# Kernel tuning notes

Hardware: AMD Instinct MI355X
Metric: run time of the kernel (lower is better)

Reference implementation:

```python
import jax, jax.numpy as jnp
import numpy as np
from jax import lax


def _leaky(x):
    # LeakyReLU, negative_slope=0.1
    return jnp.where(x > 0, x, 0.1 * x)


def _conv(x, w, pad, groups=1):
    # NCHW / OIHW 2D conv, stride 1
    return lax.conv_general_dilated(
        x, w, (1, 1), [(pad, pad), (pad, pad)],
        dimension_numbers=("NCHW", "OIHW", "NCHW"),
        feature_group_count=groups)


def setup_inputs() -> dict:
    key = jax.random.key(0)
    ks = jax.random.split(key, 12)
    B, C, H, W = 16, 64, 256, 256
    KS = 3

    def nrm(k, shape, fan_in):
        return jax.random.normal(k, shape, jnp.float32) / np.float32(np.sqrt(fan_in))

    return {
        "x": jax.random.normal(ks[0], (B, C, H, W), jnp.float32),
        "t": jax.random.normal(ks[1], (B, 1, 1, 1), jnp.float32),
        # t_process: 1x1 convs (1->64, 64->64), no bias -> stored as matrices
        "tW1": nrm(ks[2], (C, 1), 1),
        "tW2": nrm(ks[3], (C, C), C),
        # f_process: two 3x3 convs 64->64 with bias
        "fW1": nrm(ks[4], (C, C, KS, KS), C * KS * KS),
        "fb1": jnp.zeros((C,), jnp.float32),
        "fW2": nrm(ks[5], (C, C, KS, KS), C * KS * KS),
        "fb2": jnp.zeros((C,), jnp.float32),
        # kernel branch: 1x1 convs (1->64, 64->64*9), no bias
        "kW1": nrm(ks[6], (C, 1), 1),
        "kW2": nrm(ks[7], (C * KS * KS, C), C),
        # conv33: 3x3 conv 64->64 with bias
        "cW": nrm(ks[8], (C, C, KS, KS), C * KS * KS),
        "cb": jnp.zeros((C,), jnp.float32),
    }


def reference(x, t, tW1, tW2, fW1, fb1, fW2, fb2, kW1, kW2, cW, cb):
    b, c, h, w = x.shape
    KS = 3

    # f_process: Conv3x3 -> LeakyReLU -> Conv3x3 -> LeakyReLU
    f = _leaky(_conv(x, fW1, 1) + fb1[None, :, None, None])
    f = _leaky(_conv(f, fW2, 1) + fb2[None, :, None, None])

    # t is (b,1,1,1); 1x1 convs on it are per-sample matmuls
    ts = t.reshape(b, 1)
    # t_process: Conv1x1 -> LeakyReLU -> Conv1x1 -> Sigmoid -> (b,c,1,1)
    mv = jax.nn.sigmoid(_leaky(ts @ tW1.T) @ tW2.T).reshape(b, c, 1, 1)

    # kernel branch: Conv1x1 -> LeakyReLU -> Conv1x1 -> LeakyReLU -> (b*c,1,3,3)
    kern = _leaky(_leaky(ts @ kW1.T) @ kW2.T).reshape(b * c, 1, KS, KS)

    # per-sample-channel dynamic depthwise conv: groups = b*c
    out = _conv(f.reshape(1, b * c, h, w), kern, (KS - 1) // 2,
                groups=b * c).reshape(b, c, h, w)

    # modulation gating + residual 3x3 conv
    return out * mv + _conv(x, cW, 1) + cb[None, :, None, None]
```

## Files before the change

kernel.cpp:

```cpp
#include <hip/hip_runtime.h>
#include <cstdint>

using short8  = __attribute__((ext_vector_type(8))) short;
using short4v = __attribute__((ext_vector_type(4))) short;
using f32x16  = __attribute__((ext_vector_type(16))) float;
using float4v = __attribute__((ext_vector_type(4))) float;
typedef unsigned short ushort_t;

__device__ __forceinline__ float lrelu(float x) { return x > 0.f ? x : 0.1f * x; }

__device__ __forceinline__ ushort_t f2bf(float f) {
    union { float f; unsigned u; } v; v.f = f;
    unsigned r = (v.u + 0x7FFFu + ((v.u >> 16) & 1u)) >> 16;
    return (ushort_t)r;
}
__device__ __forceinline__ float bf2f(ushort_t b) {
    union { unsigned u; float f; } v; v.u = ((unsigned)b) << 16; return v.f;
}

__device__ __forceinline__ void gload_lds16(const ushort_t* g, ushort_t* l) {
    __builtin_amdgcn_global_load_lds(
        (const __attribute__((address_space(1))) void*)g,
        (__attribute__((address_space(3))) void*)l, 16, 0, 0);
}

__global__ void k_tiny(const float* __restrict__ t, const float* __restrict__ tW1,
                       const float* __restrict__ tW2, const float* __restrict__ kW1,
                       const float* __restrict__ kW2, float* __restrict__ ktr) {
    int b = blockIdx.x;
    int c = threadIdx.x;
    __shared__ float h1[64], g1[64];
    float ts = t[b];
    h1[c] = lrelu(ts * tW1[c]);
    g1[c] = lrelu(ts * kW1[c]);
    __syncthreads();
    float s = 0.f;
    for (int j = 0; j < 64; ++j) s = fmaf(tW2[c * 64 + j], h1[j], s);
    float mvv = 1.f / (1.f + expf(-s));
    for (int q = 0; q < 9; ++q) {
        float s2 = 0.f;
        for (int j = 0; j < 64; ++j) s2 = fmaf(kW2[(c * 9 + q) * 64 + j], g1[j], s2);
        ktr[b * 576 + q * 64 + c] = lrelu(s2) * mvv;
    }
}

__global__ void k_zrow(ushort_t* __restrict__ z) {
    int i = blockIdx.x * 256 + threadIdx.x;
    *(short8*)(z + (size_t)i * 8) = (short8)0;
}

__global__ void k_pack(const float* __restrict__ w1, const float* __restrict__ w2,
                       const float* __restrict__ w3, ushort_t* __restrict__ wp) {
    int idx = blockIdx.x * 256 + threadIdx.x;
    if (idx >= 3 * 36864) return;
    int conv = idx / 36864, r = idx % 36864;
    const float* W = conv == 0 ? w1 : (conv == 1 ? w2 : w3);
    int j = r & 7, lane = (r >> 3) & 63, ct = (r >> 9) & 1, kc = (r >> 10) & 1,
        ch = (r >> 11) & 1, t = r >> 12;
    int co = ct * 32 + (lane & 31);
    int ci = ch * 32 + kc * 16 + (lane >> 5) * 8 + j;
    wp[idx] = f2bf(W[(co * 64 + ci) * 9 + t]);
}

__global__ __launch_bounds__(256) void k_tr(const float* __restrict__ x,
                                            ushort_t* __restrict__ xbf) {
    int bid = blockIdx.x;
    int h = bid & 255, b = bid >> 8;
    int t = threadIdx.x;
    for (int it = 0; it < 8; ++it) {
        int idx = t + it * 256;
        int g = idx & 7, w = idx >> 3;
        const float* src = x + (((size_t)(b * 64 + g * 8) * 256 + h) * 256 + w);
        short8 v;
#pragma unroll
        for (int j = 0; j < 8; ++j) v[j] = (short)f2bf(src[(size_t)j * 65536]);
        *(short8*)(xbf + (((size_t)(b * 256 + h) * 256 + w) * 64 + g * 8)) = v;
    }
}

template <bool LEAKY, int OMODE>
__global__ __launch_bounds__(256, 3) void k_conv(const ushort_t* __restrict__ in,
                                                 const ushort_t* __restrict__ zv,
                                                 const ushort_t* __restrict__ wp,
                                                 const float* __restrict__ bias,
                                                 void* __restrict__ outp) {
    __shared__ __align__(16) ushort_t xs[3136 * 8];
    const int tid = threadIdx.x;
    const int lane = tid & 63;
    const int wv = tid >> 6;
    const unsigned bid = blockIdx.x;
    const unsigned L = (bid & 7u) * 512u + (bid >> 3);
    const int h = L & 255, b = L >> 8;
    const int l31 = lane & 31, lhi = lane >> 5;
    const int pw0 = wv * 64;

    const ushort_t* rb0 = (h > 0)   ? in + ((size_t)(b * 256 + h - 1)) * 16384 : zv;
    const ushort_t* rb1 =             in + ((size_t)(b * 256 + h)) * 16384;
    const ushort_t* rb2 = (h < 255) ? in + ((size_t)(b * 256 + h + 1)) * 16384 : zv;

    f32x16 acc[2][2];
#pragma unroll
    for (int a = 0; a < 2; ++a)
#pragma unroll
        for (int c = 0; c < 2; ++c) acc[a][c] = (f32x16)0.0f;

    for (int ch = 0; ch < 2; ++ch) {
        __syncthreads();
#pragma unroll
        for (int it = 0; it < 13; ++it) {
            int base = it * 256 + wv * 64;
            if (base < 3120) {
                int S = base + lane;
                S = S < 3120 ? S : 3119;
                int r = (S >= 2080) ? 2 : (S >= 1040 ? 1 : 0);
                int rem = S - r * 1040;
                int m = rem >> 3, sl = rem & 7;
                int sp = sl ^ (m & 7);
                int p = 2 * m + (sp >> 2), g = sp & 3;
                int ws = p - 1;
                bool edge = (unsigned)ws >= 256u;
                const ushort_t* rp = (r == 0) ? rb0 : (r == 1 ? rb1 : rb2);
                const ushort_t* src =
                    edge ? zv : (rp + ws * 64 + ch * 32 + g * 8);
                gload_lds16(src, xs + (size_t)base * 8);
            }
        }
        asm volatile("s_waitcnt vmcnt(0)" ::: "memory");
        __syncthreads();

#pragma unroll
        for (int t = 0; t < 9; ++t) {
            const int dw = t % 3;
#pragma unroll
            for (int kc = 0; kc < 2; ++kc) {
                const ushort_t* wpf = wp + (((((t * 2 + ch) * 2 + kc) * 2) * 64 + lane) * 8);
                short8 a0 = *(const short8*)(wpf);
                short8 a1 = *(const short8*)(wpf + 512);
                const int g = kc * 2 + lhi;
                const int rr = t / 3;
#pragma unroll
                for (int pt = 0; pt < 2; ++pt) {
                    int p = pw0 + pt * 32 + l31 + dw;
                    int slot = ((p & 1) * 4 + g) ^ ((p >> 1) & 7);
                    short8 bf = *(const short8*)(xs + (((size_t)rr * 130 + (p >> 1)) * 8 + slot) * 8);
                    acc[0][pt] = __builtin_amdgcn_mfma_f32_32x32x16_bf16(a0, bf, acc[0][pt], 0, 0, 0);
                    acc[1][pt] = __builtin_amdgcn_mfma_f32_32x32x16_bf16(a1, bf, acc[1][pt], 0, 0, 0);
                }
            }
        }
    }

    const int co_b = 4 * lhi;
    if (OMODE == 0) {
        ushort_t* outb = (ushort_t*)outp + ((size_t)(b * 256 + h)) * 16384;
#pragma unroll
        for (int ct = 0; ct < 2; ++ct)
#pragma unroll
            for (int pt = 0; pt < 2; ++pt) {
                int pix = pw0 + pt * 32 + l31;
                ushort_t* po = outb + (size_t)pix * 64 + ct * 32 + co_b;
#pragma unroll
                for (int q = 0; q < 4; ++q) {
                    float4v bv = *(const float4v*)(bias + ct * 32 + co_b + 8 * q);
                    short4v sv;
#pragma unroll
                    for (int m = 0; m < 4; ++m) {
                        float v = acc[ct][pt][q * 4 + m] + bv[m];
                        if (LEAKY) v = lrelu(v);
                        sv[m] = (short)f2bf(v);
                    }
                    *(short4v*)(po + 8 * q) = sv;
                }
            }
    } else if (OMODE == 1) {
        ushort_t* pb = (ushort_t*)outp + (((size_t)b * 64) << 16) + h * 256;
#pragma unroll
        for (int ct = 0; ct < 2; ++ct)
#pragma unroll
            for (int pt = 0; pt < 2; ++pt) {
                int pix = pw0 + pt * 32 + l31;
#pragma unroll
                for (int q = 0; q < 4; ++q) {
                    float4v bv = *(const float4v*)(bias + ct * 32 + co_b + 8 * q);
#pragma unroll
                    for (int m = 0; m < 4; ++m) {
                        int c = ct * 32 + co_b + 8 * q + m;
                        float v = acc[ct][pt][q * 4 + m] + bv[m];
                        if (LEAKY) v = lrelu(v);
                        pb[((size_t)c << 16) + pix] = f2bf(v);
                    }
                }
            }
    } else {
        float* pb = (float*)outp + (((size_t)b * 64) << 16) + h * 256;
#pragma unroll
        for (int ct = 0; ct < 2; ++ct)
#pragma unroll
            for (int pt = 0; pt < 2; ++pt) {
                int pix = pw0 + pt * 32 + l31;
#pragma unroll
                for (int q = 0; q < 4; ++q) {
                    float4v bv = *(const float4v*)(bias + ct * 32 + co_b + 8 * q);
#pragma unroll
                    for (int m = 0; m < 4; ++m) {
                        int c = ct * 32 + co_b + 8 * q + m;
                        float v = acc[ct][pt][q * 4 + m] + bv[m];
                        if (LEAKY) v = lrelu(v);
                        pb[((size_t)c << 16) + pix] = v;
                    }
                }
            }
    }
}

__global__ __launch_bounds__(256) void k_fin(const ushort_t* __restrict__ f2,
                                             const float* __restrict__ ktr,
                                             float* __restrict__ out) {
    __shared__ __align__(16) ushort_t s[10 * 272];
    const unsigned bid = blockIdx.x;
    const unsigned L = (bid & 7u) * 4096u + (bid >> 3);
    const int hb = L & 31, c = (L >> 5) & 63, b = L >> 11;
    const int h0 = hb * 8;
    const int w = threadIdx.x;

    const ushort_t* f2c = f2 + (((size_t)(b * 64 + c)) << 16);
    for (int i = w; i < 320; i += 256) {
        int r = i >> 5, seg = i & 31;
        int hs = h0 - 1 + r;
        short8 v = (short8)0;
        if ((unsigned)hs < 256u) v = *(const short8*)(f2c + hs * 256 + seg * 8);
        *(short8*)(&s[r * 272 + 8 + seg * 8]) = v;
        if (seg == 0) s[r * 272 + 7] = 0;
        if (seg == 31) s[r * 272 + 264] = 0;
    }
    __syncthreads();

    float kv[9];
#pragma unroll
    for (int t9 = 0; t9 < 9; ++t9) kv[t9] = ktr[b * 576 + t9 * 64 + c];

    float lv[10], cv[10], rv[10];
#pragma unroll
    for (int r = 0; r < 10; ++r) {
        lv[r] = bf2f(s[r * 272 + 7 + w]);
        cv[r] = bf2f(s[r * 272 + 8 + w]);
        rv[r] = bf2f(s[r * 272 + 9 + w]);
    }

    float* ob = out + (((size_t)(b * 64 + c)) << 16) + h0 * 256 + w;
#pragma unroll
    for (int rr = 0; rr < 8; ++rr) {
        float dwv = 0.f;
#pragma unroll
        for (int r3 = 0; r3 < 3; ++r3) {
            dwv = fmaf(kv[r3 * 3 + 0], lv[rr + r3], dwv);
            dwv = fmaf(kv[r3 * 3 + 1], cv[rr + r3], dwv);
            dwv = fmaf(kv[r3 * 3 + 2], rv[rr + r3], dwv);
        }
        float* po = ob + rr * 256;
        *po = *po + dwv;
    }
}

extern "C" void kernel_launch(void* const* d_in, const int* in_sizes, int n_in,
                              void* d_out, int out_size, void* d_ws, size_t ws_size,
                              hipStream_t stream) {
    const float* x   = (const float*)d_in[0];
    const float* t   = (const float*)d_in[1];
    const float* tW1 = (const float*)d_in[2];
    const float* tW2 = (const float*)d_in[3];
    const float* fW1 = (const float*)d_in[4];
    const float* fb1 = (const float*)d_in[5];
    const float* fW2 = (const float*)d_in[6];
    const float* fb2 = (const float*)d_in[7];
    const float* kW1 = (const float*)d_in[8];
    const float* kW2 = (const float*)d_in[9];
    const float* cW  = (const float*)d_in[10];
    const float* cb  = (const float*)d_in[11];

    char* ws = (char*)d_ws;
    float*    ktr  = (float*)ws;
    ushort_t* wp   = (ushort_t*)(ws + 65536);
    ushort_t* zv   = (ushort_t*)(ws + 294912);
    ushort_t* xbf  = (ushort_t*)(ws + (512u << 10));
    ushort_t* f2n  = (ushort_t*)(ws + (512u << 10) + ((size_t)128 << 20));
    ushort_t* f1bf = (ushort_t*)d_out;
    float*    out  = (float*)d_out;

    k_tiny<<<dim3(16), dim3(64), 0, stream>>>(t, tW1, tW2, kW1, kW2, ktr);
    k_zrow<<<dim3(8), dim3(256), 0, stream>>>(zv);
    k_pack<<<dim3((3 * 36864 + 255) / 256), dim3(256), 0, stream>>>(fW1, fW2, cW, wp);
    k_tr<<<dim3(4096), dim3(256), 0, stream>>>(x, xbf);

    k_conv<true, 0><<<dim3(4096), dim3(256), 0, stream>>>(xbf, zv, wp, fb1, (void*)f1bf);
    k_conv<true, 1><<<dim3(4096), dim3(256), 0, stream>>>(f1bf, zv, wp + 36864, fb2, (void*)f2n);
    k_conv<false, 2><<<dim3(4096), dim3(256), 0, stream>>>(xbf, zv, wp + 2 * 36864, cb, (void*)out);
    k_fin<<<dim3(32768), dim3(256), 0, stream>>>(f2n, ktr, out);
}
```

Measured before the change: 673.9 us.

## Fuse first f-conv and residual conv into one kernel sharing input tile

The first f_process conv and the residual conv33 both read the same bf16 input x, so they are merged into one kernel that stages the input tile in LDS once and runs both weight sets' MFMAs against it. This removes one full kernel launch and one full pass of input loads. The price is doubled accumulator registers (32 more f32x16 worth), which may lower occupancy under the launch bound of 3 blocks per SM or cause spills. Buffers are reassigned so f1 goes to workspace and f2 reuses the xbf buffer, since out now receives the residual early.

```diff
diff --git a/kernel.cpp b/kernel.cpp
--- a/kernel.cpp
+++ b/kernel.cpp
@@ -78,12 +78,11 @@
     }
 }
 
-template <bool LEAKY, int OMODE>
-__global__ __launch_bounds__(256, 3) void k_conv(const ushort_t* __restrict__ in,
-                                                 const ushort_t* __restrict__ zv,
-                                                 const ushort_t* __restrict__ wp,
-                                                 const float* __restrict__ bias,
-                                                 void* __restrict__ outp) {
+__global__ __launch_bounds__(256, 3) void k_conv13(
+    const ushort_t* __restrict__ in, const ushort_t* __restrict__ zv,
+    const ushort_t* __restrict__ wpa, const ushort_t* __restrict__ wpc,
+    const float* __restrict__ ba, const float* __restrict__ bc,
+    ushort_t* __restrict__ f1out, float* __restrict__ cres) {
     __shared__ __align__(16) ushort_t xs[3136 * 8];
     const int tid = threadIdx.x;
     const int lane = tid & 63;
@@ -98,11 +97,11 @@
     const ushort_t* rb1 =             in + ((size_t)(b * 256 + h)) * 16384;
     const ushort_t* rb2 = (h < 255) ? in + ((size_t)(b * 256 + h + 1)) * 16384 : zv;
 
-    f32x16 acc[2][2];
+    f32x16 accA[2][2], accC[2][2];
 #pragma unroll
     for (int a = 0; a < 2; ++a)
 #pragma unroll
-        for (int c = 0; c < 2; ++c) acc[a][c] = (f32x16)0.0f;
+        for (int c = 0; c < 2; ++c) { accA[a][c] = (f32x16)0.0f; accC[a][c] = (f32x16)0.0f; }
 
     for (int ch = 0; ch < 2; ++ch) {
         __syncthreads();
@@ -120,8 +119,7 @@
                 int ws = p - 1;
                 bool edge = (unsigned)ws >= 256u;
                 const ushort_t* rp = (r == 0) ? rb0 : (r == 1 ? rb1 : rb2);
-                const ushort_t* src =
-                    edge ? zv : (rp + ws * 64 + ch * 32 + g * 8);
+                const ushort_t* src = edge ? zv : (rp + ws * 64 + ch * 32 + g * 8);
                 gload_lds16(src, xs + (size_t)base * 8);
             }
         }
@@ -131,13 +129,129 @@
 #pragma unroll
         for (int t = 0; t < 9; ++t) {
             const int dw = t % 3;
+            const int rr = t / 3;
+#pragma unroll
+            for (int kc = 0; kc < 2; ++kc) {
+                const int off = ((((t * 2 + ch) * 2 + kc) * 2) * 64 + lane) * 8;
+                short8 a0 = *(const short8*)(wpa + off);
+                short8 a1 = *(const short8*)(wpa + off + 512);
+                short8 c0 = *(const short8*)(wpc + off);
+                short8 c1 = *(const short8*)(wpc + off + 512);
+                const int g = kc * 2 + lhi;
+#pragma unroll
+                for (int pt = 0; pt < 2; ++pt) {
+                    int p = pw0 + pt * 32 + l31 + dw;
+                    int slot = ((p & 1) * 4 + g) ^ ((p >> 1) & 7);
+                    short8 bf = *(const short8*)(xs + (((size_t)rr * 130 + (p >> 1)) * 8 + slot) * 8);
+                    accA[0][pt] = __builtin_amdgcn_mfma_f32_32x32x16_bf16(a0, bf, accA[0][pt], 0, 0, 0);
+                    accA[1][pt] = __builtin_amdgcn_mfma_f32_32x32x16_bf16(a1, bf, accA[1][pt], 0, 0, 0);
+                    accC[0][pt] = __builtin_amdgcn_mfma_f32_32x32x16_bf16(c0, bf, accC[0][pt], 0, 0, 0);
+                    accC[1][pt] = __builtin_amdgcn_mfma_f32_32x32x16_bf16(c1, bf, accC[1][pt], 0, 0, 0);
+                }
+            }
+        }
+    }
+
+    const int co_b = 4 * lhi;
+    {
+        ushort_t* outb = f1out + ((size_t)(b * 256 + h)) * 16384;
+#pragma unroll
+        for (int ct = 0; ct < 2; ++ct)
+#pragma unroll
+            for (int pt = 0; pt < 2; ++pt) {
+                int pix = pw0 + pt * 32 + l31;
+                ushort_t* po = outb + (size_t)pix * 64 + ct * 32 + co_b;
+#pragma unroll
+                for (int q = 0; q < 4; ++q) {
+                    float4v bv = *(const float4v*)(ba + ct * 32 + co_b + 8 * q);
+                    short4v sv;
+#pragma unroll
+                    for (int m = 0; m < 4; ++m) {
+                        float v = lrelu(accA[ct][pt][q * 4 + m] + bv[m]);
+                        sv[m] = (short)f2bf(v);
+                    }
+                    *(short4v*)(po + 8 * q) = sv;
+                }
+            }
+    }
+    {
+        float* pb = cres + (((size_t)b * 64) << 16) + h * 256;
+#pragma unroll
+        for (int ct = 0; ct < 2; ++ct)
+#pragma unroll
+            for (int pt = 0; pt < 2; ++pt) {
+                int pix = pw0 + pt * 32 + l31;
+#pragma unroll
+                for (int q = 0; q < 4; ++q) {
+                    float4v bv = *(const float4v*)(bc + ct * 32 + co_b + 8 * q);
+#pragma unroll
+                    for (int m = 0; m < 4; ++m) {
+                        int c = ct * 32 + co_b + 8 * q + m;
+                        pb[((size_t)c << 16) + pix] = accC[ct][pt][q * 4 + m] + bv[m];
+                    }
+                }
+            }
+    }
+}
+
+__global__ __launch_bounds__(256, 3) void k_conv2(const ushort_t* __restrict__ in,
+                                                  const ushort_t* __restrict__ zv,
+                                                  const ushort_t* __restrict__ wp,
+                                                  const float* __restrict__ bias,
+                                                  ushort_t* __restrict__ outp) {
+    __shared__ __align__(16) ushort_t xs[3136 * 8];
+    const int tid = threadIdx.x;
+    const int lane = tid & 63;
+    const int wv = tid >> 6;
+    const unsigned bid = blockIdx.x;
+    const unsigned L = (bid & 7u) * 512u + (bid >> 3);
+    const int h = L & 255, b = L >> 8;
+    const int l31 = lane & 31, lhi = lane >> 5;
+    const int pw0 = wv * 64;
+
+    const ushort_t* rb0 = (h > 0)   ? in + ((size_t)(b * 256 + h - 1)) * 16384 : zv;
+    const ushort_t* rb1 =             in + ((size_t)(b * 256 + h)) * 16384;
+    const ushort_t* rb2 = (h < 255) ? in + ((size_t)(b * 256 + h + 1)) * 16384 : zv;
+
+    f32x16 acc[2][2];
+#pragma unroll
+    for (int a = 0; a < 2; ++a)
+#pragma unroll
+        for (int c = 0; c < 2; ++c) acc[a][c] = (f32x16)0.0f;
+
+    for (int ch = 0; ch < 2; ++ch) {
+        __syncthreads();
+#pragma unroll
+        for (int it = 0; it < 13; ++it) {
+            int base = it * 256 + wv * 64;
+            if (base < 3120) {
+                int S = base + lane;
+                S = S < 3120 ? S : 3119;
+                int r = (S >= 2080) ? 2 : (S >= 1040 ? 1 : 0);
+                int rem = S - r * 1040;
+                int m = rem >> 3, sl = rem & 7;
+                int sp = sl ^ (m & 7);
+                int p = 2 * m + (sp >> 2), g = sp & 3;
+                int ws = p - 1;
+                bool edge = (unsigned)ws >= 256u;
+                const ushort_t* rp = (r == 0) ? rb0 : (r == 1 ? rb1 : rb2);
+                const ushort_t* src = edge ? zv : (rp + ws * 64 + ch * 32 + g * 8);
+                gload_lds16(src, xs + (size_t)base * 8);
+            }
+        }
+        asm volatile("s_waitcnt vmcnt(0)" ::: "memory");
+        __syncthreads();
+
+#pragma unroll
+        for (int t = 0; t < 9; ++t) {
+            const int dw = t % 3;
+            const int rr = t / 3;
 #pragma unroll
             for (int kc = 0; kc < 2; ++kc) {
                 const ushort_t* wpf = wp + (((((t * 2 + ch) * 2 + kc) * 2) * 64 + lane) * 8);
                 short8 a0 = *(const short8*)(wpf);
                 short8 a1 = *(const short8*)(wpf + 512);
                 const int g = kc * 2 + lhi;
-                const int rr = t / 3;
 #pragma unroll
                 for (int pt = 0; pt < 2; ++pt) {
                     int p = pw0 + pt * 32 + l31 + dw;
@@ -151,66 +265,23 @@
     }
 
     const int co_b = 4 * lhi;
-    if (OMODE == 0) {
-        ushort_t* outb = (ushort_t*)outp + ((size_t)(b * 256 + h)) * 16384;
-#pragma unroll
-        for (int ct = 0; ct < 2; ++ct)
-#pragma unroll
-            for (int pt = 0; pt < 2; ++pt) {
-                int pix = pw0 + pt * 32 + l31;
-                ushort_t* po = outb + (size_t)pix * 64 + ct * 32 + co_b;
-#pragma unroll
-                for (int q = 0; q < 4; ++q) {
-                    float4v bv = *(const float4v*)(bias + ct * 32 + co_b + 8 * q);
-                    short4v sv;
-#pragma unroll
-                    for (int m = 0; m < 4; ++m) {
-                        float v = acc[ct][pt][q * 4 + m] + bv[m];
-                        if (LEAKY) v = lrelu(v);
-                        sv[m] = (short)f2bf(v);
-                    }
-                    *(short4v*)(po + 8 * q) = sv;
-                }
-            }
-    } else if (OMODE == 1) {
-        ushort_t* pb = (ushort_t*)outp + (((size_t)b * 64) << 16) + h * 256;
-#pragma unroll
-        for (int ct = 0; ct < 2; ++ct)
-#pragma unroll
-            for (int pt = 0; pt < 2; ++pt) {
-                int pix = pw0 + pt * 32 + l31;
-#pragma unroll
-                for (int q = 0; q < 4; ++q) {
-                    float4v bv = *(const float4v*)(bias + ct * 32 + co_b + 8 * q);
-#pragma unroll
-                    for (int m = 0; m < 4; ++m) {
-                        int c = ct * 32 + co_b + 8 * q + m;
-                        float v = acc[ct][pt][q * 4 + m] + bv[m];
-                        if (LEAKY) v = lrelu(v);
-                        pb[((size_t)c << 16) + pix] = f2bf(v);
-                    }
-                }
-            }
-    } else {
-        float* pb = (float*)outp + (((size_t)b * 64) << 16) + h * 256;
-#pragma unroll
-        for (int ct = 0; ct < 2; ++ct)
-#pragma unroll
-            for (int pt = 0; pt < 2; ++pt) {
-                int pix = pw0 + pt * 32 + l31;
-#pragma unroll
-                for (int q = 0; q < 4; ++q) {
-                    float4v bv = *(const float4v*)(bias + ct * 32 + co_b + 8 * q);
-#pragma unroll
-                    for (int m = 0; m < 4; ++m) {
-                        int c = ct * 32 + co_b + 8 * q + m;
-                        float v = acc[ct][pt][q * 4 + m] + bv[m];
-                        if (LEAKY) v = lrelu(v);
-                        pb[((size_t)c << 16) + pix] = v;
-                    }
-                }
-            }
-    }
+    ushort_t* pb = outp + (((size_t)b * 64) << 16) + h * 256;
+#pragma unroll
+    for (int ct = 0; ct < 2; ++ct)
+#pragma unroll
+        for (int pt = 0; pt < 2; ++pt) {
+            int pix = pw0 + pt * 32 + l31;
+#pragma unroll
+            for (int q = 0; q < 4; ++q) {
+                float4v bv = *(const float4v*)(bias + ct * 32 + co_b + 8 * q);
+#pragma unroll
+                for (int m = 0; m < 4; ++m) {
+                    int c = ct * 32 + co_b + 8 * q + m;
+                    float v = lrelu(acc[ct][pt][q * 4 + m] + bv[m]);
+                    pb[((size_t)c << 16) + pix] = f2bf(v);
+                }
+            }
+        }
 }
 
 __global__ __launch_bounds__(256) void k_fin(const ushort_t* __restrict__ f2,
@@ -283,8 +354,8 @@
     ushort_t* wp   = (ushort_t*)(ws + 65536);
     ushort_t* zv   = (ushort_t*)(ws + 294912);
     ushort_t* xbf  = (ushort_t*)(ws + (512u << 10));
-    ushort_t* f2n  = (ushort_t*)(ws + (512u << 10) + ((size_t)128 << 20));
-    ushort_t* f1bf = (ushort_t*)d_out;
+    ushort_t* f1bf = (ushort_t*)(ws + (512u << 10) + ((size_t)128 << 20));
+    ushort_t* f2n  = xbf;
     float*    out  = (float*)d_out;
 
     k_tiny<<<dim3(16), dim3(64), 0, stream>>>(t, tW1, tW2, kW1, kW2, ktr);
@@ -292,8 +363,8 @@
     k_pack<<<dim3((3 * 36864 + 255) / 256), dim3(256), 0, stream>>>(fW1, fW2, cW, wp);
     k_tr<<<dim3(4096), dim3(256), 0, stream>>>(x, xbf);
 
-    k_conv<true, 0><<<dim3(4096), dim3(256), 0, stream>>>(xbf, zv, wp, fb1, (void*)f1bf);
-    k_conv<true, 1><<<dim3(4096), dim3(256), 0, stream>>>(f1bf, zv, wp + 36864, fb2, (void*)f2n);
-    k_conv<false, 2><<<dim3(4096), dim3(256), 0, stream>>>(xbf, zv, wp + 2 * 36864, cb, (void*)out);
+    k_conv13<<<dim3(4096), dim3(256), 0, stream>>>(
+        xbf, zv, wp, wp + 2 * 36864, fb1, cb, f1bf, out);
+    k_conv2<<<dim3(4096), dim3(256), 0, stream>>>(f1bf, zv, wp + 36864, fb2, f2n);
     k_fin<<<dim3(32768), dim3(256), 0, stream>>>(f2n, ktr, out);
 }
```

Result: slower. 716.1 us (+6.3%).

## Restructure conv into 2-row blocks with LDS weights, double-buffered staging, fused depthwise

Applied to the files above, without the earlier changes.

The conv kernel now uses 512-thread blocks that each compute two output rows. All weights are staged into LDS once per block, and the input channels are split into four 16-channel chunks loaded into a double-buffered LDS ring, so global loads overlap the MFMA work. The separate depthwise/final kernel is removed and its dynamic 3x3 depthwise conv is fused into the residual conv epilogue, which reads f2 directly from global memory. The cost is roughly 140KB of dynamic LDS per block, which limits occupancy, plus uncoalesced scattered f2 reads in the epilogue.

```diff
diff --git a/kernel.cpp b/kernel.cpp
--- a/kernel.cpp
+++ b/kernel.cpp
@@ -7,6 +7,13 @@
 using float4v = __attribute__((ext_vector_type(4))) float;
 typedef unsigned short ushort_t;
 
+#define CROW 520
+#define CSLOTS 2080
+#define BSLOTS 2144
+#define BSH (BSLOTS * 8)
+#define WSH 36864
+#define DYN_LDS ((WSH + 2 * BSH) * 2)
+
 __device__ __forceinline__ float lrelu(float x) { return x > 0.f ? x : 0.1f * x; }
 
 __device__ __forceinline__ ushort_t f2bf(float f) {
@@ -23,6 +30,10 @@
         (const __attribute__((address_space(1))) void*)g,
         (__attribute__((address_space(3))) void*)l, 16, 0, 0);
 }
+
+#define VMCNT(n) asm volatile("s_waitcnt vmcnt(" #n ")" ::: "memory")
+#define RBAR() __builtin_amdgcn_s_barrier()
+#define SCHED0() __builtin_amdgcn_sched_barrier(0)
 
 __global__ void k_tiny(const float* __restrict__ t, const float* __restrict__ tW1,
                        const float* __restrict__ tW2, const float* __restrict__ kW1,
@@ -55,10 +66,10 @@
     if (idx >= 3 * 36864) return;
     int conv = idx / 36864, r = idx % 36864;
     const float* W = conv == 0 ? w1 : (conv == 1 ? w2 : w3);
-    int j = r & 7, lane = (r >> 3) & 63, ct = (r >> 9) & 1, kc = (r >> 10) & 1,
-        ch = (r >> 11) & 1, t = r >> 12;
+    int j = r & 7, lane = (r >> 3) & 63, ct = (r >> 9) & 1, chunk = (r >> 10) & 3,
+        t = r >> 12;
     int co = ct * 32 + (lane & 31);
-    int ci = ch * 32 + kc * 16 + (lane >> 5) * 8 + j;
+    int ci = chunk * 16 + (lane >> 5) * 8 + j;
     wp[idx] = f2bf(W[(co * 64 + ci) * 9 + t]);
 }
 
@@ -78,25 +89,80 @@
     }
 }
 
-template <bool LEAKY, int OMODE>
-__global__ __launch_bounds__(256, 3) void k_conv(const ushort_t* __restrict__ in,
-                                                 const ushort_t* __restrict__ zv,
-                                                 const ushort_t* __restrict__ wp,
-                                                 const float* __restrict__ bias,
-                                                 void* __restrict__ outp) {
-    __shared__ __align__(16) ushort_t xs[3136 * 8];
+#define STAGE4(chunk, bufbase)                                                   \
+    {                                                                            \
+        _Pragma("unroll")                                                        \
+        for (int i_ = 0; i_ < 5; ++i_) {                                         \
+            int base_ = wv * 260 + i_ * 64;                                      \
+            int S_ = base_ + lane;                                               \
+            S_ = S_ < CSLOTS ? S_ : CSLOTS - 1;                                  \
+            int r_ = (S_ >= 1560) ? 3 : ((S_ >= 1040) ? 2 : ((S_ >= 520) ? 1 : 0)); \
+            int rem_ = S_ - r_ * 520;                                            \
+            int mg_ = rem_ >> 3, sl_ = rem_ & 7;                                 \
+            int sp_ = sl_ ^ (mg_ & 7);                                           \
+            int p_ = mg_ * 4 + (sp_ >> 1), g_ = sp_ & 1;                         \
+            int wsx_ = p_ - 1;                                                   \
+            bool edge_ = (unsigned)wsx_ >= 256u;                                 \
+            const ushort_t* rp_ =                                                \
+                (r_ == 0) ? rb0 : ((r_ == 1) ? rb1 : ((r_ == 2) ? rb2 : rb3));   \
+            const ushort_t* src_ =                                               \
+                edge_ ? zv : (rp_ + wsx_ * 64 + (chunk)*16 + g_ * 8);            \
+            gload_lds16(src_, xs + (bufbase) + (size_t)base_ * 8);               \
+        }                                                                        \
+    }
+
+__device__ __forceinline__ void computeG(const ushort_t* __restrict__ wlds,
+                                         const ushort_t* __restrict__ xs,
+                                         int bufbase, int chunk, int lane, int pw0,
+                                         int l31, int lhi, int rbase,
+                                         f32x16 (&acc)[2][2]) {
+    __builtin_amdgcn_s_setprio(1);
+#pragma unroll
+    for (int t = 0; t < 9; ++t) {
+        const int off = ((t * 4 + chunk) * 2) * 512 + lane * 8;
+        short8 a0 = *(const short8*)(wlds + off);
+        short8 a1 = *(const short8*)(wlds + off + 512);
+        const int dwx = t % 3, rr = t / 3;
+        const int rowIdx = rbase + rr;
+#pragma unroll
+        for (int pt = 0; pt < 2; ++pt) {
+            int p = pw0 + pt * 32 + l31 + dwx;
+            int mg = p >> 2;
+            int sl = ((p & 3) * 2 + lhi) ^ (mg & 7);
+            short8 bf = *(const short8*)(
+                xs + bufbase + (size_t)(rowIdx * 520 + mg * 8 + sl) * 8);
+            acc[0][pt] = __builtin_amdgcn_mfma_f32_32x32x16_bf16(a0, bf, acc[0][pt], 0, 0, 0);
+            acc[1][pt] = __builtin_amdgcn_mfma_f32_32x32x16_bf16(a1, bf, acc[1][pt], 0, 0, 0);
+        }
+    }
+    __builtin_amdgcn_s_setprio(0);
+}
+
+template <int OMODE>
+__global__ __launch_bounds__(512, 2) void k_convG(
+    const ushort_t* __restrict__ in, const ushort_t* __restrict__ zv,
+    const ushort_t* __restrict__ wp, const float* __restrict__ bias,
+    const ushort_t* __restrict__ f2, const float* __restrict__ ktr,
+    void* __restrict__ outp) {
+    extern __shared__ char smem_raw[];
+    ushort_t* wlds = (ushort_t*)smem_raw;
+    ushort_t* xs = wlds + WSH;
+
     const int tid = threadIdx.x;
     const int lane = tid & 63;
     const int wv = tid >> 6;
     const unsigned bid = blockIdx.x;
-    const unsigned L = (bid & 7u) * 512u + (bid >> 3);
-    const int h = L & 255, b = L >> 8;
+    const unsigned L = (bid & 7u) * 256u + (bid >> 3);
+    const int h0 = (L & 127) * 2, b = L >> 7;
     const int l31 = lane & 31, lhi = lane >> 5;
-    const int pw0 = wv * 64;
-
-    const ushort_t* rb0 = (h > 0)   ? in + ((size_t)(b * 256 + h - 1)) * 16384 : zv;
-    const ushort_t* rb1 =             in + ((size_t)(b * 256 + h)) * 16384;
-    const ushort_t* rb2 = (h < 255) ? in + ((size_t)(b * 256 + h + 1)) * 16384 : zv;
+    const int pw0 = (wv & 3) * 64;
+    const int rbase = wv >> 2;
+    const int ro = h0 + rbase;
+
+    const ushort_t* rb0 = (h0 > 0)    ? in + ((size_t)(b * 256 + h0 - 1)) * 16384 : zv;
+    const ushort_t* rb1 =               in + ((size_t)(b * 256 + h0)) * 16384;
+    const ushort_t* rb2 =               in + ((size_t)(b * 256 + h0 + 1)) * 16384;
+    const ushort_t* rb3 = (h0 < 254)  ? in + ((size_t)(b * 256 + h0 + 2)) * 16384 : zv;
 
     f32x16 acc[2][2];
 #pragma unroll
@@ -104,55 +170,33 @@
 #pragma unroll
         for (int c = 0; c < 2; ++c) acc[a][c] = (f32x16)0.0f;
 
-    for (int ch = 0; ch < 2; ++ch) {
-        __syncthreads();
-#pragma unroll
-        for (int it = 0; it < 13; ++it) {
-            int base = it * 256 + wv * 64;
-            if (base < 3120) {
-                int S = base + lane;
-                S = S < 3120 ? S : 3119;
-                int r = (S >= 2080) ? 2 : (S >= 1040 ? 1 : 0);
-                int rem = S - r * 1040;
-                int m = rem >> 3, sl = rem & 7;
-                int sp = sl ^ (m & 7);
-                int p = 2 * m + (sp >> 2), g = sp & 3;
-                int ws = p - 1;
-                bool edge = (unsigned)ws >= 256u;
-                const ushort_t* rp = (r == 0) ? rb0 : (r == 1 ? rb1 : rb2);
-                const ushort_t* src =
-                    edge ? zv : (rp + ws * 64 + ch * 32 + g * 8);
-                gload_lds16(src, xs + (size_t)base * 8);
-            }
-        }
-        asm volatile("s_waitcnt vmcnt(0)" ::: "memory");
-        __syncthreads();
-
-#pragma unroll
-        for (int t = 0; t < 9; ++t) {
-            const int dw = t % 3;
-#pragma unroll
-            for (int kc = 0; kc < 2; ++kc) {
-                const ushort_t* wpf = wp + (((((t * 2 + ch) * 2 + kc) * 2) * 64 + lane) * 8);
-                short8 a0 = *(const short8*)(wpf);
-                short8 a1 = *(const short8*)(wpf + 512);
-                const int g = kc * 2 + lhi;
-                const int rr = t / 3;
-#pragma unroll
-                for (int pt = 0; pt < 2; ++pt) {
-                    int p = pw0 + pt * 32 + l31 + dw;
-                    int slot = ((p & 1) * 4 + g) ^ ((p >> 1) & 7);
-                    short8 bf = *(const short8*)(xs + (((size_t)rr * 130 + (p >> 1)) * 8 + slot) * 8);
-                    acc[0][pt] = __builtin_amdgcn_mfma_f32_32x32x16_bf16(a0, bf, acc[0][pt], 0, 0, 0);
-                    acc[1][pt] = __builtin_amdgcn_mfma_f32_32x32x16_bf16(a1, bf, acc[1][pt], 0, 0, 0);
-                }
-            }
-        }
-    }
+#pragma unroll
+    for (int i = 0; i < 9; ++i) {
+        int idx = wv * 9 + i;
+        gload_lds16(wp + (size_t)idx * 512 + lane * 8, wlds + (size_t)idx * 512);
+    }
+    STAGE4(0, 0);
+    STAGE4(1, BSH);
+    VMCNT(5);
+    RBAR(); SCHED0();
+    computeG(wlds, xs, 0, 0, lane, pw0, l31, lhi, rbase, acc);
+    RBAR();
+    STAGE4(2, 0);
+    VMCNT(5);
+    RBAR(); SCHED0();
+    computeG(wlds, xs, BSH, 1, lane, pw0, l31, lhi, rbase, acc);
+    RBAR();
+    STAGE4(3, BSH);
+    VMCNT(5);
+    RBAR(); SCHED0();
+    computeG(wlds, xs, 0, 2, lane, pw0, l31, lhi, rbase, acc);
+    VMCNT(0);
+    RBAR(); SCHED0();
+    computeG(wlds, xs, BSH, 3, lane, pw0, l31, lhi, rbase, acc);
 
     const int co_b = 4 * lhi;
     if (OMODE == 0) {
-        ushort_t* outb = (ushort_t*)outp + ((size_t)(b * 256 + h)) * 16384;
+        ushort_t* outb = (ushort_t*)outp + ((size_t)(b * 256 + ro)) * 16384;
 #pragma unroll
         for (int ct = 0; ct < 2; ++ct)
 #pragma unroll
@@ -165,15 +209,14 @@
                     short4v sv;
 #pragma unroll
                     for (int m = 0; m < 4; ++m) {
-                        float v = acc[ct][pt][q * 4 + m] + bv[m];
-                        if (LEAKY) v = lrelu(v);
+                        float v = lrelu(acc[ct][pt][q * 4 + m] + bv[m]);
                         sv[m] = (short)f2bf(v);
                     }
                     *(short4v*)(po + 8 * q) = sv;
                 }
             }
     } else if (OMODE == 1) {
-        ushort_t* pb = (ushort_t*)outp + (((size_t)b * 64) << 16) + h * 256;
+        ushort_t* pb = (ushort_t*)outp + (((size_t)b * 64) << 16) + ro * 256;
 #pragma unroll
         for (int ct = 0; ct < 2; ++ct)
 #pragma unroll
@@ -185,14 +228,13 @@
 #pragma unroll
                     for (int m = 0; m < 4; ++m) {
                         int c = ct * 32 + co_b + 8 * q + m;
-                        float v = acc[ct][pt][q * 4 + m] + bv[m];
-                        if (LEAKY) v = lrelu(v);
+                        float v = lrelu(acc[ct][pt][q * 4 + m] + bv[m]);
                         pb[((size_t)c << 16) + pix] = f2bf(v);
                     }
                 }
             }
     } else {
-        float* pb = (float*)outp + (((size_t)b * 64) << 16) + h * 256;
+        float* pb = (float*)outp + (((size_t)b * 64) << 16) + ro * 256;
 #pragma unroll
         for (int ct = 0; ct < 2; ++ct)
 #pragma unroll
@@ -200,65 +242,38 @@
                 int pix = pw0 + pt * 32 + l31;
 #pragma unroll
                 for (int q = 0; q < 4; ++q) {
-                    float4v bv = *(const float4v*)(bias + ct * 32 + co_b + 8 * q);
+                    const int cb4 = ct * 32 + co_b + 8 * q;
+                    float4v kv[9];
+#pragma unroll
+                    for (int t9 = 0; t9 < 9; ++t9)
+                        kv[t9] = *(const float4v*)(ktr + b * 576 + t9 * 64 + cb4);
+                    float4v bv = *(const float4v*)(bias + cb4);
+                    float dw4[4] = {0.f, 0.f, 0.f, 0.f};
 #pragma unroll
                     for (int m = 0; m < 4; ++m) {
-                        int c = ct * 32 + co_b + 8 * q + m;
-                        float v = acc[ct][pt][q * 4 + m] + bv[m];
-                        if (LEAKY) v = lrelu(v);
-                        pb[((size_t)c << 16) + pix] = v;
+                        const ushort_t* f2c =
+                            f2 + (((size_t)(b * 64 + cb4 + m)) << 16);
+#pragma unroll
+                        for (int rr2 = 0; rr2 < 3; ++rr2) {
+                            int hh = ro - 1 + rr2;
+                            if ((unsigned)hh >= 256u) continue;
+                            const ushort_t* fr = f2c + hh * 256;
+#pragma unroll
+                            for (int dx = 0; dx < 3; ++dx) {
+                                int wsx = pix + dx - 1;
+                                bool ok = (unsigned)wsx < 256u;
+                                float xv = ok ? bf2f(fr[ok ? wsx : 0]) : 0.f;
+                                dw4[m] = fmaf(kv[rr2 * 3 + dx][m], xv, dw4[m]);
+                            }
+                        }
+                    }
+#pragma unroll
+                    for (int m = 0; m < 4; ++m) {
+                        float v = acc[ct][pt][q * 4 + m] + bv[m] + dw4[m];
+                        pb[((size_t)(cb4 + m) << 16) + pix] = v;
                     }
                 }
             }
-    }
-}
-
-__global__ __launch_bounds__(256) void k_fin(const ushort_t* __restrict__ f2,
-                                             const float* __restrict__ ktr,
-                                             float* __restrict__ out) {
-    __shared__ __align__(16) ushort_t s[10 * 272];
-    const unsigned bid = blockIdx.x;
-    const unsigned L = (bid & 7u) * 4096u + (bid >> 3);
-    const int hb = L & 31, c = (L >> 5) & 63, b = L >> 11;
-    const int h0 = hb * 8;
-    const int w = threadIdx.x;
-
-    const ushort_t* f2c = f2 + (((size_t)(b * 64 + c)) << 16);
-    for (int i = w; i < 320; i += 256) {
-        int r = i >> 5, seg = i & 31;
-        int hs = h0 - 1 + r;
-        short8 v = (short8)0;
-        if ((unsigned)hs < 256u) v = *(const short8*)(f2c + hs * 256 + seg * 8);
-        *(short8*)(&s[r * 272 + 8 + seg * 8]) = v;
-        if (seg == 0) s[r * 272 + 7] = 0;
-        if (seg == 31) s[r * 272 + 264] = 0;
-    }
-    __syncthreads();
-
-    float kv[9];
-#pragma unroll
-    for (int t9 = 0; t9 < 9; ++t9) kv[t9] = ktr[b * 576 + t9 * 64 + c];
-
-    float lv[10], cv[10], rv[10];
-#pragma unroll
-    for (int r = 0; r < 10; ++r) {
-        lv[r] = bf2f(s[r * 272 + 7 + w]);
-        cv[r] = bf2f(s[r * 272 + 8 + w]);
-        rv[r] = bf2f(s[r * 272 + 9 + w]);
-    }
-
-    float* ob = out + (((size_t)(b * 64 + c)) << 16) + h0 * 256 + w;
-#pragma unroll
-    for (int rr = 0; rr < 8; ++rr) {
-        float dwv = 0.f;
-#pragma unroll
-        for (int r3 = 0; r3 < 3; ++r3) {
-            dwv = fmaf(kv[r3 * 3 + 0], lv[rr + r3], dwv);
-            dwv = fmaf(kv[r3 * 3 + 1], cv[rr + r3], dwv);
-            dwv = fmaf(kv[r3 * 3 + 2], rv[rr + r3], dwv);
-        }
-        float* po = ob + rr * 256;
-        *po = *po + dwv;
     }
 }
 
@@ -287,13 +302,22 @@
     ushort_t* f1bf = (ushort_t*)d_out;
     float*    out  = (float*)d_out;
 
+    hipFuncSetAttribute(reinterpret_cast<const void*>(&k_convG<0>),
+                        hipFuncAttributeMaxDynamicSharedMemorySize, DYN_LDS);
+    hipFuncSetAttribute(reinterpret_cast<const void*>(&k_convG<1>),
+                        hipFuncAttributeMaxDynamicSharedMemorySize, DYN_LDS);
+    hipFuncSetAttribute(reinterpret_cast<const void*>(&k_convG<2>),
+                        hipFuncAttributeMaxDynamicSharedMemorySize, DYN_LDS);
+
     k_tiny<<<dim3(16), dim3(64), 0, stream>>>(t, tW1, tW2, kW1, kW2, ktr);
     k_zrow<<<dim3(8), dim3(256), 0, stream>>>(zv);
     k_pack<<<dim3((3 * 36864 + 255) / 256), dim3(256), 0, stream>>>(fW1, fW2, cW, wp);
     k_tr<<<dim3(4096), dim3(256), 0, stream>>>(x, xbf);
 
-    k_conv<true, 0><<<dim3(4096), dim3(256), 0, stream>>>(xbf, zv, wp, fb1, (void*)f1bf);
-    k_conv<true, 1><<<dim3(4096), dim3(256), 0, stream>>>(f1bf, zv, wp + 36864, fb2, (void*)f2n);
-    k_conv<false, 2><<<dim3(4096), dim3(256), 0, stream>>>(xbf, zv, wp + 2 * 36864, cb, (void*)out);
-    k_fin<<<dim3(32768), dim3(256), 0, stream>>>(f2n, ktr, out);
-}
+    k_convG<0><<<dim3(2048), dim3(512), DYN_LDS, stream>>>(
+        xbf, zv, wp, fb1, nullptr, nullptr, (void*)f1bf);
+    k_convG<1><<<dim3(2048), dim3(512), DYN_LDS, stream>>>(
+        f1bf, zv, wp + 36864, fb2, nullptr, nullptr, (void*)f2n);
+    k_convG<2><<<dim3(2048), dim3(512), DYN_LDS, stream>>>(
+        xbf, zv, wp + 2 * 36864, cb, f2n, ktr, (void*)out);
+}
```

Result: slower. 1.083 ms (+60.8%).

## Double-buffer conv input staging in 16-channel chunks with preloaded weights

Applied to the files above, without the earlier changes.

The conv kernel now stages its input halo rows in four 16-channel chunks, using two LDS buffers so that the global-to-LDS loads for the next chunk overlap MFMA compute on the current one. All 9 taps of weights for a chunk are preloaded into registers, and compute runs at raised wave priority. Buffers are reordered so f2 reuses the xbf buffer, which means the residual conv now runs before the second f conv. The cost is more register pressure from holding 18 short8 weight fragments, plus manual vmcnt bookkeeping that breaks silently if the number of issued loads changes.

```diff
diff --git a/kernel.cpp b/kernel.cpp
--- a/kernel.cpp
+++ b/kernel.cpp
@@ -7,6 +7,11 @@
 using float4v = __attribute__((ext_vector_type(4))) float;
 typedef unsigned short ushort_t;
 
+#define CHUNK_ROW 520
+#define CHUNK_SLOTS 1560
+#define BUF_SLOTS 1632
+#define BUF_SHORTS (BUF_SLOTS * 8)
+
 __device__ __forceinline__ float lrelu(float x) { return x > 0.f ? x : 0.1f * x; }
 
 __device__ __forceinline__ ushort_t f2bf(float f) {
@@ -23,6 +28,11 @@
         (const __attribute__((address_space(1))) void*)g,
         (__attribute__((address_space(3))) void*)l, 16, 0, 0);
 }
+
+#define VMCNT(n) asm volatile("s_waitcnt vmcnt(" #n ")" ::: "memory")
+#define RBAR() __builtin_amdgcn_s_barrier()
+#define SCHED0() __builtin_amdgcn_sched_barrier(0)
+#define PIN() asm volatile("" ::: "memory")
 
 __global__ void k_tiny(const float* __restrict__ t, const float* __restrict__ tW1,
                        const float* __restrict__ tW2, const float* __restrict__ kW1,
@@ -55,10 +65,10 @@
     if (idx >= 3 * 36864) return;
     int conv = idx / 36864, r = idx % 36864;
     const float* W = conv == 0 ? w1 : (conv == 1 ? w2 : w3);
-    int j = r & 7, lane = (r >> 3) & 63, ct = (r >> 9) & 1, kc = (r >> 10) & 1,
-        ch = (r >> 11) & 1, t = r >> 12;
+    int j = r & 7, lane = (r >> 3) & 63, ct = (r >> 9) & 1, chunk = (r >> 10) & 3,
+        t = r >> 12;
     int co = ct * 32 + (lane & 31);
-    int ci = ch * 32 + kc * 16 + (lane >> 5) * 8 + j;
+    int ci = chunk * 16 + (lane >> 5) * 8 + j;
     wp[idx] = f2bf(W[(co * 64 + ci) * 9 + t]);
 }
 
@@ -78,13 +88,66 @@
     }
 }
 
-template <bool LEAKY, int OMODE>
-__global__ __launch_bounds__(256, 3) void k_conv(const ushort_t* __restrict__ in,
-                                                 const ushort_t* __restrict__ zv,
-                                                 const ushort_t* __restrict__ wp,
-                                                 const float* __restrict__ bias,
-                                                 void* __restrict__ outp) {
-    __shared__ __align__(16) ushort_t xs[3136 * 8];
+#define STAGE_CHUNK(chunk, bufbase)                                              \
+    {                                                                            \
+        _Pragma("unroll")                                                        \
+        for (int i_ = 0; i_ < 7; ++i_) {                                         \
+            int base_ = wv * 390 + i_ * 64;                                      \
+            int S_ = base_ + lane;                                               \
+            S_ = S_ < CHUNK_SLOTS ? S_ : CHUNK_SLOTS - 1;                        \
+            int row_ = (S_ >= 2 * CHUNK_ROW) ? 2 : (S_ >= CHUNK_ROW ? 1 : 0);    \
+            int rem_ = S_ - row_ * CHUNK_ROW;                                    \
+            int mg_ = rem_ >> 3, sl_ = rem_ & 7;                                 \
+            int sp_ = sl_ ^ (mg_ & 7);                                           \
+            int p_ = mg_ * 4 + (sp_ >> 1), g_ = sp_ & 1;                         \
+            int wsx_ = p_ - 1;                                                   \
+            bool edge_ = (unsigned)wsx_ >= 256u;                                 \
+            const ushort_t* rp_ = (row_ == 0) ? rb0 : (row_ == 1 ? rb1 : rb2);   \
+            const ushort_t* src_ =                                               \
+                edge_ ? zv : (rp_ + wsx_ * 64 + (chunk)*16 + g_ * 8);            \
+            gload_lds16(src_, xs + (bufbase) + (size_t)base_ * 8);               \
+        }                                                                        \
+    }
+
+#define LOADA(chunk)                                                             \
+    {                                                                            \
+        _Pragma("unroll")                                                        \
+        for (int t_ = 0; t_ < 9; ++t_) {                                         \
+            const ushort_t* wf_ =                                                \
+                wp + ((size_t)(t_ * 4 + (chunk)) * 2) * 512 + lane * 8;          \
+            aw[t_][0] = *(const short8*)(wf_);                                   \
+            aw[t_][1] = *(const short8*)(wf_ + 512);                             \
+        }                                                                        \
+    }
+
+#define COMPUTE(xbase)                                                           \
+    {                                                                            \
+        __builtin_amdgcn_s_setprio(1);                                           \
+        _Pragma("unroll")                                                        \
+        for (int t_ = 0; t_ < 9; ++t_) {                                         \
+            const int dwx_ = t_ % 3, rr_ = t_ / 3;                               \
+            _Pragma("unroll")                                                    \
+            for (int pt_ = 0; pt_ < 2; ++pt_) {                                  \
+                int p_ = pw0 + pt_ * 32 + l31 + dwx_;                            \
+                int mg_ = p_ >> 2;                                               \
+                int sl_ = ((p_ & 3) * 2 + lhi) ^ (mg_ & 7);                      \
+                short8 bf = *(const short8*)(                                    \
+                    xs + (xbase) + (size_t)(rr_ * CHUNK_ROW + mg_ * 8 + sl_) * 8);\
+                acc[0][pt_] = __builtin_amdgcn_mfma_f32_32x32x16_bf16(           \
+                    aw[t_][0], bf, acc[0][pt_], 0, 0, 0);                        \
+                acc[1][pt_] = __builtin_amdgcn_mfma_f32_32x32x16_bf16(           \
+                    aw[t_][1], bf, acc[1][pt_], 0, 0, 0);                        \
+            }                                                                    \
+        }                                                                        \
+        __builtin_amdgcn_s_setprio(0);                                           \
+    }
+
+template <int OMODE>
+__global__ __launch_bounds__(256, 3) void k_conv(
+    const ushort_t* __restrict__ in, const ushort_t* __restrict__ zv,
+    const ushort_t* __restrict__ wp, const float* __restrict__ bias,
+    void* __restrict__ outp) {
+    __shared__ __align__(16) ushort_t xs[2 * BUF_SHORTS];
     const int tid = threadIdx.x;
     const int lane = tid & 63;
     const int wv = tid >> 6;
@@ -104,51 +167,32 @@
 #pragma unroll
         for (int c = 0; c < 2; ++c) acc[a][c] = (f32x16)0.0f;
 
-    for (int ch = 0; ch < 2; ++ch) {
-        __syncthreads();
-#pragma unroll
-        for (int it = 0; it < 13; ++it) {
-            int base = it * 256 + wv * 64;
-            if (base < 3120) {
-                int S = base + lane;
-                S = S < 3120 ? S : 3119;
-                int r = (S >= 2080) ? 2 : (S >= 1040 ? 1 : 0);
-                int rem = S - r * 1040;
-                int m = rem >> 3, sl = rem & 7;
-                int sp = sl ^ (m & 7);
-                int p = 2 * m + (sp >> 2), g = sp & 3;
-                int ws = p - 1;
-                bool edge = (unsigned)ws >= 256u;
-                const ushort_t* rp = (r == 0) ? rb0 : (r == 1 ? rb1 : rb2);
-                const ushort_t* src =
-                    edge ? zv : (rp + ws * 64 + ch * 32 + g * 8);
-                gload_lds16(src, xs + (size_t)base * 8);
-            }
-        }
-        asm volatile("s_waitcnt vmcnt(0)" ::: "memory");
-        __syncthreads();
-
-#pragma unroll
-        for (int t = 0; t < 9; ++t) {
-            const int dw = t % 3;
-#pragma unroll
-            for (int kc = 0; kc < 2; ++kc) {
-                const ushort_t* wpf = wp + (((((t * 2 + ch) * 2 + kc) * 2) * 64 + lane) * 8);
-                short8 a0 = *(const short8*)(wpf);
-                short8 a1 = *(const short8*)(wpf + 512);
-                const int g = kc * 2 + lhi;
-                const int rr = t / 3;
-#pragma unroll
-                for (int pt = 0; pt < 2; ++pt) {
-                    int p = pw0 + pt * 32 + l31 + dw;
-                    int slot = ((p & 1) * 4 + g) ^ ((p >> 1) & 7);
-                    short8 bf = *(const short8*)(xs + (((size_t)rr * 130 + (p >> 1)) * 8 + slot) * 8);
-                    acc[0][pt] = __builtin_amdgcn_mfma_f32_32x32x16_bf16(a0, bf, acc[0][pt], 0, 0, 0);
-                    acc[1][pt] = __builtin_amdgcn_mfma_f32_32x32x16_bf16(a1, bf, acc[1][pt], 0, 0, 0);
-                }
-            }
-        }
-    }
+    short8 aw[9][2];
+
+    LOADA(0);
+    PIN();
+    STAGE_CHUNK(0, 0);
+    STAGE_CHUNK(1, BUF_SHORTS);
+    VMCNT(7);
+    RBAR(); SCHED0();
+    COMPUTE(0);
+    LOADA(1);
+    PIN();
+    VMCNT(18);
+    RBAR(); SCHED0();
+    STAGE_CHUNK(2, 0);
+    COMPUTE(BUF_SHORTS);
+    LOADA(2);
+    PIN();
+    VMCNT(18);
+    RBAR(); SCHED0();
+    STAGE_CHUNK(3, BUF_SHORTS);
+    COMPUTE(0);
+    LOADA(3);
+    PIN();
+    VMCNT(18);
+    RBAR(); SCHED0();
+    COMPUTE(BUF_SHORTS);
 
     const int co_b = 4 * lhi;
     if (OMODE == 0) {
@@ -165,8 +209,7 @@
                     short4v sv;
 #pragma unroll
                     for (int m = 0; m < 4; ++m) {
-                        float v = acc[ct][pt][q * 4 + m] + bv[m];
-                        if (LEAKY) v = lrelu(v);
+                        float v = lrelu(acc[ct][pt][q * 4 + m] + bv[m]);
                         sv[m] = (short)f2bf(v);
                     }
                     *(short4v*)(po + 8 * q) = sv;
@@ -185,8 +228,7 @@
 #pragma unroll
                     for (int m = 0; m < 4; ++m) {
                         int c = ct * 32 + co_b + 8 * q + m;
-                        float v = acc[ct][pt][q * 4 + m] + bv[m];
-                        if (LEAKY) v = lrelu(v);
+                        float v = lrelu(acc[ct][pt][q * 4 + m] + bv[m]);
                         pb[((size_t)c << 16) + pix] = f2bf(v);
                     }
                 }
@@ -204,9 +246,7 @@
 #pragma unroll
                     for (int m = 0; m < 4; ++m) {
                         int c = ct * 32 + co_b + 8 * q + m;
-                        float v = acc[ct][pt][q * 4 + m] + bv[m];
-                        if (LEAKY) v = lrelu(v);
-                        pb[((size_t)c << 16) + pix] = v;
+                        pb[((size_t)c << 16) + pix] = acc[ct][pt][q * 4 + m] + bv[m];
                     }
                 }
             }
@@ -283,8 +323,8 @@
     ushort_t* wp   = (ushort_t*)(ws + 65536);
     ushort_t* zv   = (ushort_t*)(ws + 294912);
     ushort_t* xbf  = (ushort_t*)(ws + (512u << 10));
-    ushort_t* f2n  = (ushort_t*)(ws + (512u << 10) + ((size_t)128 << 20));
-    ushort_t* f1bf = (ushort_t*)d_out;
+    ushort_t* f1bf = (ushort_t*)(ws + (512u << 10) + ((size_t)128 << 20));
+    ushort_t* f2n  = xbf;
     float*    out  = (float*)d_out;
 
     k_tiny<<<dim3(16), dim3(64), 0, stream>>>(t, tW1, tW2, kW1, kW2, ktr);
@@ -292,8 +332,8 @@
     k_pack<<<dim3((3 * 36864 + 255) / 256), dim3(256), 0, stream>>>(fW1, fW2, cW, wp);
     k_tr<<<dim3(4096), dim3(256), 0, stream>>>(x, xbf);
 
-    k_conv<true, 0><<<dim3(4096), dim3(256), 0, stream>>>(xbf, zv, wp, fb1, (void*)f1bf);
-    k_conv<true, 1><<<dim3(4096), dim3(256), 0, stream>>>(f1bf, zv, wp + 36864, fb2, (void*)f2n);
-    k_conv<false, 2><<<dim3(4096), dim3(256), 0, stream>>>(xbf, zv, wp + 2 * 36864, cb, (void*)out);
+    k_conv<0><<<dim3(4096), dim3(256), 0, stream>>>(xbf, zv, wp, fb1, (void*)f1bf);
+    k_conv<2><<<dim3(4096), dim3(256), 0, stream>>>(xbf, zv, wp + 2 * 36864, cb, (void*)out);
+    k_conv<1><<<dim3(4096), dim3(256), 0, stream>>>(f1bf, zv, wp + 36864, fb2, (void*)f2n);
     k_fin<<<dim3(32768), dim3(256), 0, stream>>>(f2n, ktr, out);
 }
```

Result: slower. 888.7 us (+31.9%).
